# Performance work log

Hardware: AMD Instinct MI355X
Metric: run time of the kernel (lower is better)

Reference implementation:

```python
import jax, jax.numpy as jnp
import numpy as np

B, S, D, H = 4, 4096, 1024, 1024


def log_g(x):
    # where(x >= 0, log(relu(x) + 0.5), -softplus(-x)); relu(x)+0.5 >= 0.5 so log is safe
    return jnp.where(x >= 0, jnp.log(jax.nn.relu(x) + 0.5), -jax.nn.softplus(-x))


def setup_inputs() -> dict:
    key = jax.random.key(0)
    ks = jax.random.split(key, 8)
    scale = 1.0 / np.sqrt(D)
    return {
        "x_t": jax.random.normal(ks[0], (B, S, D), dtype=jnp.float32),
        "pre_h": jax.random.normal(ks[1], (B, 1, H), dtype=jnp.float32),
        "W_f": jax.random.uniform(ks[2], (H, D), jnp.float32, -scale, scale),
        "b_f": jax.random.uniform(ks[3], (H,), jnp.float32, -scale, scale),
        "W_i": jax.random.uniform(ks[4], (H, D), jnp.float32, -scale, scale),
        "b_i": jax.random.uniform(ks[5], (H,), jnp.float32, -scale, scale),
        "W_h": jax.random.uniform(ks[6], (H, D), jnp.float32, -scale, scale),
        "b_h": jax.random.uniform(ks[7], (H,), jnp.float32, -scale, scale),
    }


def reference(x_t, pre_h, W_f, b_f, W_i, b_i, W_h, b_h):
    sp = jax.nn.softplus
    f_pre = jnp.einsum("bsd,hd->bsh", x_t, W_f) + b_f
    i_pre = jnp.einsum("bsd,hd->bsh", x_t, W_i) + b_i
    h_pre = jnp.einsum("bsd,hd->bsh", x_t, W_h) + b_h

    diff = sp(-f_pre) - sp(-i_pre)
    log_f = -sp(diff)        # (B, S, H)
    log_i = -sp(-diff)       # (B, S, H)

    log_h0 = log_g(pre_h)                 # (B, 1, H)
    log_tilde_h = log_g(h_pre)            # (B, S, H)
    log_values = jnp.concatenate([log_h0, log_i + log_tilde_h], axis=1)  # (B, S+1, H)

    # parallel_scan_log: pad cumsum at END of seq dim (as in source: F.pad(..., (0,0,0,1)))
    a_star = jnp.pad(jnp.cumsum(log_f, axis=1), ((0, 0), (0, 1), (0, 0)))  # (B, S+1, H)
    log_h0_plus_b_star = jax.lax.cumlogsumexp(log_values - a_star, axis=1)
    log_h = a_star + log_h0_plus_b_star
    return jnp.exp(log_h)[:, 1:]  # (B, S, H)
```

## Files before the change

### kernel.cpp

```cpp
#include <hip/hip_runtime.h>
#include <hip/hip_bf16.h>
#include <math.h>

#define B_DIM 4
#define S_DIM 4096
#define K_DIM 1024
#define H_DIM 1024
#define M_DIM (B_DIM * S_DIM)

#define BMT 128
#define BNT 64
#define KT_ITERS (K_DIM / 32)

#define NCHUNK 64
#define CLEN (S_DIM / NCHUNK)

typedef __attribute__((ext_vector_type(8))) _Float16 f16x8;
typedef __attribute__((ext_vector_type(4))) _Float16 f16x4;
typedef __attribute__((ext_vector_type(4))) float f32x4;

__device__ __forceinline__ float sp_f(float x) {
    return fmaxf(x, 0.0f) + __logf(1.0f + __expf(-fabsf(x)));
}
__device__ __forceinline__ float log_g_f(float x) {
    return (x >= 0.0f) ? __logf(x + 0.5f) : -sp_f(-x);
}
__device__ __forceinline__ float logaddexp_f(float a, float b) {
    float m = fmaxf(a, b);
    return m + __logf(1.0f + __expf(-fabsf(a - b)));
}
__device__ __forceinline__ float exp_sat(float x) {
    return __expf(fminf(x, 85.0f));
}

__device__ __forceinline__ void gl_lds16(const void* g, void* l) {
    __builtin_amdgcn_global_load_lds(
        (const __attribute__((address_space(1))) unsigned int*)g,
        (__attribute__((address_space(3))) unsigned int*)l, 16, 0, 0);
}

__global__ __launch_bounds__(256) void conv_f16(
    const float* __restrict__ src, _Float16* __restrict__ dst, int n4)
{
    int i = blockIdx.x * 256 + threadIdx.x;
    if (i >= n4) return;
    float4 v = ((const float4*)src)[i];
    f16x4 o = {(_Float16)v.x, (_Float16)v.y, (_Float16)v.z, (_Float16)v.w};
    ((f16x4*)dst)[i] = o;
}

__global__ __launch_bounds__(256, 3) void gemm3(
    const _Float16* __restrict__ xh,
    const _Float16* __restrict__ wh,
    const float* __restrict__ bfp, const float* __restrict__ bip,
    const float* __restrict__ bhp,
    _Float16* __restrict__ lf_out, _Float16* __restrict__ w_out)
{
    __shared__ __align__(16) char smemA[20480];
    __shared__ __align__(16) char smemB[20480];

    const int tid = threadIdx.x;
    const int lane = tid & 63;
    const int wv = tid >> 6;
    const int wm = wv >> 1;
    const int wn = wv & 1;

    const int row0 = blockIdx.y * BMT;
    const int col0 = blockIdx.x * BNT;

    const int arow = tid & 127, akq = tid >> 7;
    unsigned ga0 = (unsigned)(((row0 + arow) * K_DIM + akq * 8) * 2);
    const int brow = tid & 63, bkq = tid >> 6;
    unsigned gb0 = (unsigned)(((0 * H_DIM + col0 + brow) * K_DIM + bkq * 8) * 2);
    unsigned gb1 = (unsigned)(((1 * H_DIM + col0 + brow) * K_DIM + bkq * 8) * 2);
    unsigned gb2 = (unsigned)(((2 * H_DIM + col0 + brow) * K_DIM + bkq * 8) * 2);

    const char* __restrict__ px = (const char*)xh;
    const char* __restrict__ pw = (const char*)wh;

    int aoff[4], boff[2];
#pragma unroll
    for (int mi = 0; mi < 4; ++mi)
        aoff[mi] = ((lane >> 4) << 11) + ((wm * 64 + mi * 16 + (lane & 15)) << 4);
#pragma unroll
    for (int nj = 0; nj < 2; ++nj)
        boff[nj] = ((lane >> 4) << 10) + ((wn * 32 + nj * 16 + (lane & 15)) << 4);

    f32x4 acc[3][4][2];
#pragma unroll
    for (int g = 0; g < 3; ++g)
#pragma unroll
        for (int mi = 0; mi < 4; ++mi)
#pragma unroll
            for (int nj = 0; nj < 2; ++nj)
                acc[g][mi][nj] = (f32x4){0.f, 0.f, 0.f, 0.f};

#define PREFETCH(nb) do { \
    gl_lds16(px + ga0,      (nb) + tid * 16); \
    gl_lds16(px + ga0 + 32, (nb) + 4096 + tid * 16); \
    gl_lds16(pw + gb0, (nb) + 8192  + tid * 16); \
    gl_lds16(pw + gb1, (nb) + 12288 + tid * 16); \
    gl_lds16(pw + gb2, (nb) + 16384 + tid * 16); \
    ga0 += 64; gb0 += 64; gb1 += 64; gb2 += 64; \
    __builtin_amdgcn_sched_barrier(0); } while (0)

#define COMPUTE(sb) do { \
    f16x8 a_[4]; \
    _Pragma("unroll") \
    for (int mi = 0; mi < 4; ++mi) \
        a_[mi] = *(const f16x8*)((sb) + aoff[mi]); \
    _Pragma("unroll") \
    for (int g = 0; g < 3; ++g) { \
        const char* bb_ = (sb) + 8192 + g * 4096; \
        f16x8 b0_ = *(const f16x8*)(bb_ + boff[0]); \
        f16x8 b1_ = *(const f16x8*)(bb_ + boff[1]); \
        __builtin_amdgcn_s_setprio(1); \
        _Pragma("unroll") \
        for (int mi = 0; mi < 4; ++mi) { \
            acc[g][mi][0] = __builtin_amdgcn_mfma_f32_16x16x32_f16(a_[mi], b0_, acc[g][mi][0], 0, 0, 0); \
            acc[g][mi][1] = __builtin_amdgcn_mfma_f32_16x16x32_f16(a_[mi], b1_, acc[g][mi][1], 0, 0, 0); \
        } \
        __builtin_amdgcn_s_setprio(0); \
    } } while (0)

    PREFETCH(smemA);
    __syncthreads();

#pragma unroll 1
    for (int it = 0; it < (KT_ITERS - 2) / 2; ++it) {
        PREFETCH(smemB);
        COMPUTE(smemA);
        __syncthreads();
        PREFETCH(smemA);
        COMPUTE(smemB);
        __syncthreads();
    }
    PREFETCH(smemB);
    COMPUTE(smemA);
    __syncthreads();
    COMPUTE(smemB);

#undef PREFETCH
#undef COMPUTE

    int nidx[2];
    float bfv[2], biv[2], bhv[2];
#pragma unroll
    for (int nj = 0; nj < 2; ++nj) {
        nidx[nj] = col0 + wn * 32 + nj * 16 + (lane & 15);
        bfv[nj] = bfp[nidx[nj]];
        biv[nj] = bip[nidx[nj]];
        bhv[nj] = bhp[nidx[nj]];
    }
#pragma unroll
    for (int mi = 0; mi < 4; ++mi) {
#pragma unroll
        for (int r = 0; r < 4; ++r) {
            int m = row0 + wm * 64 + mi * 16 + ((lane >> 4) << 2) + r;
#pragma unroll
            for (int nj = 0; nj < 2; ++nj) {
                float f_pre = acc[0][mi][nj][r] + bfv[nj];
                float i_pre = acc[1][mi][nj][r] + biv[nj];
                float h_pre = acc[2][mi][nj][r] + bhv[nj];
                float diff = sp_f(-f_pre) - sp_f(-i_pre);
                float lfv = -sp_f(diff);
                float wv_ = -sp_f(-diff) + log_g_f(h_pre);
                size_t o = (size_t)m * H_DIM + nidx[nj];
                lf_out[o] = (_Float16)lfv;
                w_out[o] = (_Float16)wv_;
            }
        }
    }
}

__global__ __launch_bounds__(256) void scan_pass_a(
    const _Float16* __restrict__ lf, const _Float16* __restrict__ w,
    float2* __restrict__ agg)
{
    int tid = blockIdx.x * blockDim.x + threadIdx.x;
    int h = tid & (H_DIM - 1);
    int b = (tid >> 10) & (B_DIM - 1);
    int q = tid >> 12;

    int tstart = q * CLEN + 1;
    int tend = (q == NCHUNK - 1) ? (S_DIM - 1) : (q * CLEN + CLEN);

    size_t idx = (size_t)(b * S_DIM + tstart) * H_DIM + h;
    float c = 0.0f, r = -INFINITY;
    for (int t = tstart; t <= tend; ++t) {
        c += (float)lf[idx];
        r = logaddexp_f(r, (float)w[idx - H_DIM] - c);
        idx += H_DIM;
    }
    agg[(size_t)(b * H_DIM + h) * NCHUNK + q] = make_float2(c, r);
}

__global__ __launch_bounds__(256) void scan_pass_b(
    const _Float16* __restrict__ lf, const float* __restrict__ preh,
    const float2* __restrict__ agg, float2* __restrict__ prefix)
{
    int col = blockIdx.x * blockDim.x + threadIdx.x;
    int h = col & (H_DIM - 1);
    int b = col >> 10;

    float lf0 = (float)lf[(size_t)(b * S_DIM) * H_DIM + h];
    float C = lf0;
    float R = log_g_f(preh[b * H_DIM + h]) - lf0;
    for (int q = 0; q < NCHUNK; ++q) {
        prefix[(size_t)col * NCHUNK + q] = make_float2(C, R);
        float2 a = agg[(size_t)col * NCHUNK + q];
        float Rn = logaddexp_f(R, a.y - C);
        C += a.x;
        R = Rn;
    }
}

__global__ __launch_bounds__(256) void scan_pass_c(
    const _Float16* __restrict__ lf, const _Float16* __restrict__ w,
    const float2* __restrict__ prefix, float* __restrict__ out)
{
    int tid = blockIdx.x * blockDim.x + threadIdx.x;
    int h = tid & (H_DIM - 1);
    int b = (tid >> 10) & (B_DIM - 1);
    int q = tid >> 12;

    float2 p = prefix[(size_t)(b * H_DIM + h) * NCHUNK + q];
    float C = p.x, R = p.y;

    int tstart = q * CLEN + 1;
    int tend = (q == NCHUNK - 1) ? (S_DIM - 1) : (q * CLEN + CLEN);

    size_t idx = (size_t)(b * S_DIM + tstart) * H_DIM + h;
    for (int t = tstart; t <= tend; ++t) {
        C += (float)lf[idx];
        R = logaddexp_f(R, (float)w[idx - H_DIM] - C);
        out[idx - H_DIM] = exp_sat(C + R);
        idx += H_DIM;
    }
    if (q == NCHUNK - 1) {
        R = logaddexp_f(R, (float)w[idx - H_DIM]);
        out[idx - H_DIM] = exp_sat(R);
    }
}

extern "C" void kernel_launch(void* const* d_in, const int* in_sizes, int n_in,
                              void* d_out, int out_size, void* d_ws, size_t ws_size,
                              hipStream_t stream) {
    const float* x    = (const float*)d_in[0];
    const float* preh = (const float*)d_in[1];
    const float* Wf   = (const float*)d_in[2];
    const float* bf   = (const float*)d_in[3];
    const float* Wi   = (const float*)d_in[4];
    const float* bi   = (const float*)d_in[5];
    const float* Wh   = (const float*)d_in[6];
    const float* bh   = (const float*)d_in[7];
    float* out = (float*)d_out;

    _Float16* xh = (_Float16*)d_ws;
    _Float16* wh = xh + (size_t)M_DIM * K_DIM;
    _Float16* lf = wh + (size_t)3 * H_DIM * K_DIM;
    _Float16* wbuf = lf + (size_t)M_DIM * H_DIM;
    float2* agg = (float2*)(wbuf + (size_t)M_DIM * H_DIM);
    float2* prefix = agg + (size_t)B_DIM * H_DIM * NCHUNK;

    conv_f16<<<(M_DIM * K_DIM / 4) / 256, 256, 0, stream>>>(x, xh, M_DIM * K_DIM / 4);
    conv_f16<<<(H_DIM * K_DIM / 4) / 256, 256, 0, stream>>>(Wf, wh, H_DIM * K_DIM / 4);
    conv_f16<<<(H_DIM * K_DIM / 4) / 256, 256, 0, stream>>>(
        Wi, wh + (size_t)H_DIM * K_DIM, H_DIM * K_DIM / 4);
    conv_f16<<<(H_DIM * K_DIM / 4) / 256, 256, 0, stream>>>(
        Wh, wh + (size_t)2 * H_DIM * K_DIM, H_DIM * K_DIM / 4);

    gemm3<<<dim3(H_DIM / BNT, M_DIM / BMT), 256, 0, stream>>>(
        xh, wh, bf, bi, bh, lf, wbuf);

    scan_pass_a<<<(B_DIM * H_DIM * NCHUNK) / 256, 256, 0, stream>>>(lf, wbuf, agg);
    scan_pass_b<<<(B_DIM * H_DIM) / 256, 256, 0, stream>>>(lf, preh, agg, prefix);
    scan_pass_c<<<(B_DIM * H_DIM * NCHUNK) / 256, 256, 0, stream>>>(lf, wbuf, prefix, out);
}
```

Baseline: 388.6 us.

## Triple-buffer GEMM LDS pipeline and vectorize scan passes four columns per thread

The GEMM moves from a double-buffered LDS pipeline to a three-slot ring. It uses explicit vmcnt waits and raw barriers, so two tile loads stay in flight during compute, and it drops the s_setprio hints. Occupancy drops from 3 to 2 blocks per CU because of the added LDS. Scan passes A and C now handle four adjacent hidden columns per thread, with f16x4 loads and float4 stores and a quarter as many threads. This cuts memory instructions but lowers scan parallelism.

```diff
diff --git a/kernel.cpp b/kernel.cpp
--- a/kernel.cpp
+++ b/kernel.cpp
@@ -49,15 +49,16 @@
     ((f16x4*)dst)[i] = o;
 }
 
-__global__ __launch_bounds__(256, 3) void gemm3(
+__global__ __launch_bounds__(256, 2) void gemm3(
     const _Float16* __restrict__ xh,
     const _Float16* __restrict__ wh,
     const float* __restrict__ bfp, const float* __restrict__ bip,
     const float* __restrict__ bhp,
     _Float16* __restrict__ lf_out, _Float16* __restrict__ w_out)
 {
-    __shared__ __align__(16) char smemA[20480];
-    __shared__ __align__(16) char smemB[20480];
+    __shared__ __align__(16) char smem0[20480];
+    __shared__ __align__(16) char smem1[20480];
+    __shared__ __align__(16) char smem2[20480];
 
     const int tid = threadIdx.x;
     const int lane = tid & 63;
@@ -114,34 +115,36 @@
         const char* bb_ = (sb) + 8192 + g * 4096; \
         f16x8 b0_ = *(const f16x8*)(bb_ + boff[0]); \
         f16x8 b1_ = *(const f16x8*)(bb_ + boff[1]); \
-        __builtin_amdgcn_s_setprio(1); \
         _Pragma("unroll") \
         for (int mi = 0; mi < 4; ++mi) { \
             acc[g][mi][0] = __builtin_amdgcn_mfma_f32_16x16x32_f16(a_[mi], b0_, acc[g][mi][0], 0, 0, 0); \
             acc[g][mi][1] = __builtin_amdgcn_mfma_f32_16x16x32_f16(a_[mi], b1_, acc[g][mi][1], 0, 0, 0); \
         } \
-        __builtin_amdgcn_s_setprio(0); \
     } } while (0)
 
-    PREFETCH(smemA);
-    __syncthreads();
+#define SLOT_WAIT do { \
+    asm volatile("s_waitcnt vmcnt(5) lgkmcnt(0)" ::: "memory"); \
+    __builtin_amdgcn_s_barrier(); } while (0)
+
+    PREFETCH(smem0);
+    PREFETCH(smem1);
+    asm volatile("s_waitcnt vmcnt(5)" ::: "memory");
+    __builtin_amdgcn_s_barrier();
 
 #pragma unroll 1
-    for (int it = 0; it < (KT_ITERS - 2) / 2; ++it) {
-        PREFETCH(smemB);
-        COMPUTE(smemA);
-        __syncthreads();
-        PREFETCH(smemA);
-        COMPUTE(smemB);
-        __syncthreads();
-    }
-    PREFETCH(smemB);
-    COMPUTE(smemA);
-    __syncthreads();
-    COMPUTE(smemB);
+    for (int it = 0; it < (KT_ITERS - 2) / 3; ++it) {
+        PREFETCH(smem2); COMPUTE(smem0); SLOT_WAIT;
+        PREFETCH(smem0); COMPUTE(smem1); SLOT_WAIT;
+        PREFETCH(smem1); COMPUTE(smem2); SLOT_WAIT;
+    }
+    COMPUTE(smem0);
+    asm volatile("s_waitcnt vmcnt(0) lgkmcnt(0)" ::: "memory");
+    __builtin_amdgcn_s_barrier();
+    COMPUTE(smem1);
 
 #undef PREFETCH
 #undef COMPUTE
+#undef SLOT_WAIT
 
     int nidx[2];
     float bfv[2], biv[2], bhv[2];
@@ -178,21 +181,31 @@
     float2* __restrict__ agg)
 {
     int tid = blockIdx.x * blockDim.x + threadIdx.x;
-    int h = tid & (H_DIM - 1);
-    int b = (tid >> 10) & (B_DIM - 1);
-    int q = tid >> 12;
+    int hq = tid & (H_DIM / 4 - 1);
+    int b = (tid >> 8) & (B_DIM - 1);
+    int q = tid >> 10;
+    int h0 = hq * 4;
 
     int tstart = q * CLEN + 1;
     int tend = (q == NCHUNK - 1) ? (S_DIM - 1) : (q * CLEN + CLEN);
 
-    size_t idx = (size_t)(b * S_DIM + tstart) * H_DIM + h;
-    float c = 0.0f, r = -INFINITY;
+    size_t idx = (size_t)(b * S_DIM + tstart) * H_DIM + h0;
+    float c[4] = {0.f, 0.f, 0.f, 0.f};
+    float r[4] = {-INFINITY, -INFINITY, -INFINITY, -INFINITY};
+#pragma unroll 4
     for (int t = tstart; t <= tend; ++t) {
-        c += (float)lf[idx];
-        r = logaddexp_f(r, (float)w[idx - H_DIM] - c);
+        f16x4 lv = *(const f16x4*)(lf + idx);
+        f16x4 wv = *(const f16x4*)(w + idx - H_DIM);
+#pragma unroll
+        for (int j = 0; j < 4; ++j) {
+            c[j] += (float)lv[j];
+            r[j] = logaddexp_f(r[j], (float)wv[j] - c[j]);
+        }
         idx += H_DIM;
     }
-    agg[(size_t)(b * H_DIM + h) * NCHUNK + q] = make_float2(c, r);
+#pragma unroll
+    for (int j = 0; j < 4; ++j)
+        agg[(size_t)(b * H_DIM + h0 + j) * NCHUNK + q] = make_float2(c[j], r[j]);
 }
 
 __global__ __launch_bounds__(256) void scan_pass_b(
@@ -220,26 +233,42 @@
     const float2* __restrict__ prefix, float* __restrict__ out)
 {
     int tid = blockIdx.x * blockDim.x + threadIdx.x;
-    int h = tid & (H_DIM - 1);
-    int b = (tid >> 10) & (B_DIM - 1);
-    int q = tid >> 12;
-
-    float2 p = prefix[(size_t)(b * H_DIM + h) * NCHUNK + q];
-    float C = p.x, R = p.y;
+    int hq = tid & (H_DIM / 4 - 1);
+    int b = (tid >> 8) & (B_DIM - 1);
+    int q = tid >> 10;
+    int h0 = hq * 4;
+
+    float C[4], R[4];
+#pragma unroll
+    for (int j = 0; j < 4; ++j) {
+        float2 p = prefix[(size_t)(b * H_DIM + h0 + j) * NCHUNK + q];
+        C[j] = p.x; R[j] = p.y;
+    }
 
     int tstart = q * CLEN + 1;
     int tend = (q == NCHUNK - 1) ? (S_DIM - 1) : (q * CLEN + CLEN);
 
-    size_t idx = (size_t)(b * S_DIM + tstart) * H_DIM + h;
+    size_t idx = (size_t)(b * S_DIM + tstart) * H_DIM + h0;
+#pragma unroll 4
     for (int t = tstart; t <= tend; ++t) {
-        C += (float)lf[idx];
-        R = logaddexp_f(R, (float)w[idx - H_DIM] - C);
-        out[idx - H_DIM] = exp_sat(C + R);
+        f16x4 lv = *(const f16x4*)(lf + idx);
+        f16x4 wv = *(const f16x4*)(w + idx - H_DIM);
+        float4 ov;
+        C[0] += (float)lv[0]; R[0] = logaddexp_f(R[0], (float)wv[0] - C[0]); ov.x = exp_sat(C[0] + R[0]);
+        C[1] += (float)lv[1]; R[1] = logaddexp_f(R[1], (float)wv[1] - C[1]); ov.y = exp_sat(C[1] + R[1]);
+        C[2] += (float)lv[2]; R[2] = logaddexp_f(R[2], (float)wv[2] - C[2]); ov.z = exp_sat(C[2] + R[2]);
+        C[3] += (float)lv[3]; R[3] = logaddexp_f(R[3], (float)wv[3] - C[3]); ov.w = exp_sat(C[3] + R[3]);
+        *(float4*)(out + idx - H_DIM) = ov;
         idx += H_DIM;
     }
     if (q == NCHUNK - 1) {
-        R = logaddexp_f(R, (float)w[idx - H_DIM]);
-        out[idx - H_DIM] = exp_sat(R);
+        f16x4 wv = *(const f16x4*)(w + idx - H_DIM);
+        float4 ov;
+        ov.x = exp_sat(logaddexp_f(R[0], (float)wv[0]));
+        ov.y = exp_sat(logaddexp_f(R[1], (float)wv[1]));
+        ov.z = exp_sat(logaddexp_f(R[2], (float)wv[2]));
+        ov.w = exp_sat(logaddexp_f(R[3], (float)wv[3]));
+        *(float4*)(out + idx - H_DIM) = ov;
     }
 }
 
@@ -273,7 +302,7 @@
     gemm3<<<dim3(H_DIM / BNT, M_DIM / BMT), 256, 0, stream>>>(
         xh, wh, bf, bi, bh, lf, wbuf);
 
-    scan_pass_a<<<(B_DIM * H_DIM * NCHUNK) / 256, 256, 0, stream>>>(lf, wbuf, agg);
+    scan_pass_a<<<(B_DIM * H_DIM * NCHUNK / 4) / 256, 256, 0, stream>>>(lf, wbuf, agg);
     scan_pass_b<<<(B_DIM * H_DIM) / 256, 256, 0, stream>>>(lf, preh, agg, prefix);
-    scan_pass_c<<<(B_DIM * H_DIM * NCHUNK) / 256, 256, 0, stream>>>(lf, wbuf, prefix, out);
-}
+    scan_pass_c<<<(B_DIM * H_DIM * NCHUNK / 4) / 256, 256, 0, stream>>>(lf, wbuf, prefix, out);
+}
```

Result: no change. 386.6 us (-0.5%).
